# Performance work log

Measured on AMD Instinct MI355X. Metric: run time of the kernel, lower is better.

## Reference

```python
import jax, jax.numpy as jnp
import numpy as np

B, A_DIM, B_DIM, HID = 256, 128, 128, 512


def setup_inputs() -> dict:
    key = jax.random.key(0)
    ks = jax.random.split(key, 11)
    s = 0.02
    return {
        "x": jax.random.normal(ks[0], (B, A_DIM), jnp.float32),
        "y": jax.random.normal(ks[1], (B, B_DIM), jnp.float32),
        # First Linear(A+B -> H), weight split into x-part and y-part
        "Wx": jax.random.normal(ks[2], (A_DIM, HID), jnp.float32) * s,
        "Wy": jax.random.normal(ks[3], (B_DIM, HID), jnp.float32) * s,
        "b0": jax.random.normal(ks[4], (HID,), jnp.float32) * s,
        "W1": jax.random.normal(ks[5], (HID, HID), jnp.float32) * s,
        "b1": jax.random.normal(ks[6], (HID,), jnp.float32) * s,
        "W2": jax.random.normal(ks[7], (HID, HID), jnp.float32) * s,
        "b2": jax.random.normal(ks[8], (HID,), jnp.float32) * s,
        "W3": jax.random.normal(ks[9], (HID, 1), jnp.float32) * s,
        "b3": jax.random.normal(ks[10], (1,), jnp.float32) * s,
    }


def reference(x, y, Wx, Wy, b0, W1, b1, W2, b2, W3, b3):
    # Original: pair (i,j) of the *transposed* output scores f(concat(x[i], y[j])).
    # First Linear over the concat decomposes into x- and y-projections summed
    # by broadcast, avoiding the O(B^2 * (A+B)) tiled concat tensor.
    hx = x @ Wx                      # [B, H]
    hy = y @ Wy                      # [B, H]
    h = jax.nn.relu(hx[:, None, :] + hy[None, :, :] + b0)  # [B, B, H]
    h = jax.nn.relu(h @ W1 + b1)     # [B, B, H]
    h = jax.nn.relu(h @ W2 + b2)     # [B, B, H]
    scores = h @ W3 + b3             # [B, B, 1]
    return scores[..., 0]            # [B, B], out[i,j] = f(x[i], y[j])
```

## Files before the change

kernel.cpp:

```cpp
#include <hip/hip_runtime.h>
#include <hip/hip_bf16.h>

#define BSZ 256
#define ADIM 128
#define HID 512
#define MT 64
#define LDH 520

typedef __attribute__((ext_vector_type(8))) short short8;
typedef __attribute__((ext_vector_type(4))) float float4_t;

__device__ inline short f32_to_bf16_bits(float f) {
    union { float f; unsigned u; } v; v.f = f;
    unsigned u = v.u;
    unsigned r = u + 0x7FFFu + ((u >> 16) & 1u);
    return (short)(r >> 16);
}
__device__ inline float bf16_bits_to_f32(short s) {
    union { unsigned u; float f; } v;
    v.u = ((unsigned)(unsigned short)s) << 16;
    return v.f;
}

__global__ __launch_bounds__(512) void prep_kernel(
        const float* __restrict__ x, const float* __restrict__ y,
        const float* __restrict__ Wx, const float* __restrict__ Wy,
        const float* __restrict__ b0, const float* __restrict__ W1,
        const float* __restrict__ W2,
        float* __restrict__ hx, float* __restrict__ hy,
        short* __restrict__ W1p, short* __restrict__ W2p) {
    __shared__ float lds[64 * 65];
    const int tid = threadIdx.x;
    const int bid = blockIdx.x;

    if (bid < 128) {
        const bool isX = bid < 64;
        const int i0 = (isX ? bid : bid - 64) * 4;
        const float* src = isX ? x : y;
        const float* W   = isX ? Wx : Wy;
        float* dst       = isX ? hx : hy;

        lds[tid] = src[i0 * ADIM + tid];
        __syncthreads();

        const int h = tid;
        float s0 = 0.f, s1 = 0.f, s2 = 0.f, s3 = 0.f;
        const float* wcol = W + h;
        #pragma unroll 8
        for (int k = 0; k < ADIM; ++k) {
            float w = wcol[k * HID];
            s0 = fmaf(lds[k], w, s0);
            s1 = fmaf(lds[ADIM + k], w, s1);
            s2 = fmaf(lds[2 * ADIM + k], w, s2);
            s3 = fmaf(lds[3 * ADIM + k], w, s3);
        }
        float bb = isX ? b0[h] : 0.f;
        dst[(i0 + 0) * HID + h] = s0 + bb;
        dst[(i0 + 1) * HID + h] = s1 + bb;
        dst[(i0 + 2) * HID + h] = s2 + bb;
        dst[(i0 + 3) * HID + h] = s3 + bb;
    } else {
        const int tb = bid - 128;
        const bool is1 = tb < 64;
        const int t8 = is1 ? tb : tb - 64;
        const float* Wsrc = is1 ? W1 : W2;
        short* Wdst = is1 ? W1p : W2p;
        const int k0 = (t8 >> 3) * 64;
        const int n0 = (t8 & 7) * 64;

        #pragma unroll
        for (int i = 0; i < 8; ++i) {
            int r = (tid >> 6) + i * 8;
            int c = tid & 63;
            lds[c * 65 + r] = Wsrc[(k0 + r) * HID + n0 + c];
        }
        __syncthreads();

        const int local_s = tid >> 8;
        const int g_local = (tid >> 6) & 3;
        const int lane    = tid & 63;
        const int quad    = lane >> 4;
        const int lq      = lane & 15;
        const int s_glob  = (t8 >> 3) * 2 + local_s;
        const int g_glob  = (t8 & 7) * 4 + g_local;

        const float* srcp = lds + (g_local * 16 + lq) * 65 + local_s * 32 + quad * 8;
        short8 v;
        #pragma unroll
        for (int j = 0; j < 8; ++j) v[j] = f32_to_bf16_bits(srcp[j]);
        *(short8*)(Wdst + ((s_glob * 32 + g_glob) * 64 + lane) * 8) = v;
    }
}

__device__ __forceinline__ void gemm_layer(short* __restrict__ hs,
                                           const short* __restrict__ Wp,
                                           const float* __restrict__ bias,
                                           int wave, int lane) {
    const int quad = lane >> 4;
    const int lq = lane & 15;
    const int n0 = wave * 64;

    float4_t acc[4][4];
    #pragma unroll
    for (int mi = 0; mi < 4; ++mi)
        #pragma unroll
        for (int ni = 0; ni < 4; ++ni)
            acc[mi][ni] = (float4_t){0.f, 0.f, 0.f, 0.f};

    const short* pb = Wp + wave * 2048 + lane * 8;
    const short* abase = hs + lq * LDH + quad * 8;

    short8 bf[2][4];
    #pragma unroll
    for (int ni = 0; ni < 4; ++ni)
        bf[0][ni] = *(const short8*)(pb + ni * 512);

    #pragma unroll
    for (int s = 0; s < 16; ++s) {
        const int cur = s & 1;
        if (s < 15) {
            #pragma unroll
            for (int ni = 0; ni < 4; ++ni)
                bf[cur ^ 1][ni] = *(const short8*)(pb + (s + 1) * 16384 + ni * 512);
        }
        short8 af[4];
        #pragma unroll
        for (int mi = 0; mi < 4; ++mi)
            af[mi] = *(const short8*)(abase + mi * 16 * LDH + s * 32);
        #pragma unroll
        for (int mi = 0; mi < 4; ++mi)
            #pragma unroll
            for (int ni = 0; ni < 4; ++ni)
                acc[mi][ni] = __builtin_amdgcn_mfma_f32_16x16x32_bf16(
                    af[mi], bf[cur][ni], acc[mi][ni], 0, 0, 0);
    }

    float bv[4];
    #pragma unroll
    for (int ni = 0; ni < 4; ++ni) bv[ni] = bias[n0 + ni * 16 + lq];

    __syncthreads();

    #pragma unroll
    for (int ni = 0; ni < 4; ++ni) {
        #pragma unroll
        for (int mi = 0; mi < 4; ++mi) {
            #pragma unroll
            for (int r = 0; r < 4; ++r) {
                float v = acc[mi][ni][r] + bv[ni];
                v = fmaxf(v, 0.f);
                hs[(mi * 16 + quad * 4 + r) * LDH + n0 + ni * 16 + lq] = f32_to_bf16_bits(v);
            }
        }
    }
    __syncthreads();
}

__global__ __launch_bounds__(512, 4) void critic_kernel(
    const float* __restrict__ hx, const float* __restrict__ hy,
    const short* __restrict__ W1p, const short* __restrict__ W2p,
    const float* __restrict__ b1, const float* __restrict__ b2,
    const float* __restrict__ W3, const float* __restrict__ b3,
    float* __restrict__ out) {
    __shared__ short hs[MT * LDH];
    __shared__ float psum[512];

    const int tid = threadIdx.x;
    const int wave = tid >> 6;
    const int lane = tid & 63;

    const int i0 = (blockIdx.x >> 5) * 8;
    const int j0 = (blockIdx.x & 31) * 8;

    #pragma unroll
    for (int e = tid; e < MT * 64; e += 512) {
        int r = e >> 6;
        int ko = (e & 63) * 8;
        int ti = r >> 3, tj = r & 7;
        const float4_t* px = (const float4_t*)(hx + (i0 + ti) * HID + ko);
        const float4_t* py = (const float4_t*)(hy + (j0 + tj) * HID + ko);
        float4_t a0 = px[0], a1 = px[1];
        float4_t c0 = py[0], c1 = py[1];
        short8 v;
        #pragma unroll
        for (int u = 0; u < 4; ++u) v[u]     = f32_to_bf16_bits(fmaxf(a0[u] + c0[u], 0.f));
        #pragma unroll
        for (int u = 0; u < 4; ++u) v[4 + u] = f32_to_bf16_bits(fmaxf(a1[u] + c1[u], 0.f));
        *(short8*)(hs + r * LDH + ko) = v;
    }
    __syncthreads();

    gemm_layer(hs, W1p, b1, wave, lane);
    gemm_layer(hs, W2p, b2, wave, lane);

    {
        int r = tid >> 3;
        int oc = (tid & 7) * 64;
        const short* hrow = hs + r * LDH + oc;
        float s = 0.f;
        #pragma unroll
        for (int k = 0; k < 64; k += 8) {
            short8 v = *(const short8*)(hrow + k);
            #pragma unroll
            for (int u = 0; u < 8; ++u)
                s = fmaf(bf16_bits_to_f32(v[u]), W3[oc + k + u], s);
        }
        psum[tid] = s;
    }
    __syncthreads();
    if (tid < 64) {
        float s = b3[0];
        #pragma unroll
        for (int o = 0; o < 8; ++o) s += psum[tid * 8 + o];
        int ti = tid >> 3, tj = tid & 7;
        out[(i0 + ti) * BSZ + (j0 + tj)] = s;
    }
}

extern "C" void kernel_launch(void* const* d_in, const int* in_sizes, int n_in,
                              void* d_out, int out_size, void* d_ws, size_t ws_size,
                              hipStream_t stream) {
    const float* x  = (const float*)d_in[0];
    const float* y  = (const float*)d_in[1];
    const float* Wx = (const float*)d_in[2];
    const float* Wy = (const float*)d_in[3];
    const float* b0 = (const float*)d_in[4];
    const float* W1 = (const float*)d_in[5];
    const float* b1 = (const float*)d_in[6];
    const float* W2 = (const float*)d_in[7];
    const float* b2 = (const float*)d_in[8];
    const float* W3 = (const float*)d_in[9];
    const float* b3 = (const float*)d_in[10];
    float* out = (float*)d_out;

    char* ws = (char*)d_ws;
    float* hx  = (float*)(ws);
    float* hy  = (float*)(ws + 512 * 1024);
    short* W1p = (short*)(ws + 1024 * 1024);
    short* W2p = (short*)(ws + 1536 * 1024);

    prep_kernel<<<256, 512, 0, stream>>>(x, y, Wx, Wy, b0, W1, W2, hx, hy, W1p, W2p);
    critic_kernel<<<1024, 512, 0, stream>>>(hx, hy, W1p, W2p, b1, b2, W3, b3, out);
}
```

Baseline: 147.8 us.

## Use packed bf16 converts, MFMA final projection, and setprio around MFMA blocks

Replaces the software bf16 rounding with the hardware v_cvt_pk_bf16_f32 instruction in the hidden-state build and the GEMM epilogues. The W3 dot product now runs on MFMA, using a B operand that is non-zero only in column 0, and the partial sums are written to a padded psum array. The MFMA bursts are wrapped in s_setprio, the weight-prefetch pointer is strength-reduced, and prep reads x/y directly instead of staging them in LDS. Together these aim to cut VALU work in the epilogues. The final projection now multiplies W3 in bf16, which lowers its precision.

```diff
diff --git a/kernel.cpp b/kernel.cpp
--- a/kernel.cpp
+++ b/kernel.cpp
@@ -9,6 +9,7 @@
 
 typedef __attribute__((ext_vector_type(8))) short short8;
 typedef __attribute__((ext_vector_type(4))) float float4_t;
+typedef __attribute__((ext_vector_type(4))) unsigned uint4_t;
 
 __device__ inline short f32_to_bf16_bits(float f) {
     union { float f; unsigned u; } v; v.f = f;
@@ -16,10 +17,11 @@
     unsigned r = u + 0x7FFFu + ((u >> 16) & 1u);
     return (short)(r >> 16);
 }
-__device__ inline float bf16_bits_to_f32(short s) {
-    union { unsigned u; float f; } v;
-    v.u = ((unsigned)(unsigned short)s) << 16;
-    return v.f;
+
+__device__ __forceinline__ unsigned cvt_pk_bf16(float lo, float hi) {
+    unsigned r;
+    asm("v_cvt_pk_bf16_f32 %0, %1, %2" : "=v"(r) : "v"(lo), "v"(hi));
+    return r;
 }
 
 __global__ __launch_bounds__(512) void prep_kernel(
@@ -40,19 +42,17 @@
         const float* W   = isX ? Wx : Wy;
         float* dst       = isX ? hx : hy;
 
-        lds[tid] = src[i0 * ADIM + tid];
-        __syncthreads();
-
         const int h = tid;
+        const float* r0 = src + i0 * ADIM;
         float s0 = 0.f, s1 = 0.f, s2 = 0.f, s3 = 0.f;
         const float* wcol = W + h;
         #pragma unroll 8
         for (int k = 0; k < ADIM; ++k) {
             float w = wcol[k * HID];
-            s0 = fmaf(lds[k], w, s0);
-            s1 = fmaf(lds[ADIM + k], w, s1);
-            s2 = fmaf(lds[2 * ADIM + k], w, s2);
-            s3 = fmaf(lds[3 * ADIM + k], w, s3);
+            s0 = fmaf(r0[k], w, s0);
+            s1 = fmaf(r0[ADIM + k], w, s1);
+            s2 = fmaf(r0[2 * ADIM + k], w, s2);
+            s3 = fmaf(r0[3 * ADIM + k], w, s3);
         }
         float bb = isX ? b0[h] : 0.f;
         dst[(i0 + 0) * HID + h] = s0 + bb;
@@ -115,24 +115,29 @@
     for (int ni = 0; ni < 4; ++ni)
         bf[0][ni] = *(const short8*)(pb + ni * 512);
 
+    const short* ps = pb + 16384;
+
     #pragma unroll
     for (int s = 0; s < 16; ++s) {
         const int cur = s & 1;
         if (s < 15) {
             #pragma unroll
             for (int ni = 0; ni < 4; ++ni)
-                bf[cur ^ 1][ni] = *(const short8*)(pb + (s + 1) * 16384 + ni * 512);
+                bf[cur ^ 1][ni] = *(const short8*)(ps + ni * 512);
+            ps += 16384;
         }
         short8 af[4];
         #pragma unroll
         for (int mi = 0; mi < 4; ++mi)
             af[mi] = *(const short8*)(abase + mi * 16 * LDH + s * 32);
+        __builtin_amdgcn_s_setprio(1);
         #pragma unroll
         for (int mi = 0; mi < 4; ++mi)
             #pragma unroll
             for (int ni = 0; ni < 4; ++ni)
                 acc[mi][ni] = __builtin_amdgcn_mfma_f32_16x16x32_bf16(
                     af[mi], bf[cur][ni], acc[mi][ni], 0, 0, 0);
+        __builtin_amdgcn_s_setprio(0);
     }
 
     float bv[4];
@@ -145,12 +150,18 @@
     for (int ni = 0; ni < 4; ++ni) {
         #pragma unroll
         for (int mi = 0; mi < 4; ++mi) {
-            #pragma unroll
-            for (int r = 0; r < 4; ++r) {
-                float v = acc[mi][ni][r] + bv[ni];
-                v = fmaxf(v, 0.f);
-                hs[(mi * 16 + quad * 4 + r) * LDH + n0 + ni * 16 + lq] = f32_to_bf16_bits(v);
-            }
+            float v0 = fmaxf(acc[mi][ni][0] + bv[ni], 0.f);
+            float v1 = fmaxf(acc[mi][ni][1] + bv[ni], 0.f);
+            float v2 = fmaxf(acc[mi][ni][2] + bv[ni], 0.f);
+            float v3 = fmaxf(acc[mi][ni][3] + bv[ni], 0.f);
+            unsigned p01 = cvt_pk_bf16(v0, v1);
+            unsigned p23 = cvt_pk_bf16(v2, v3);
+            unsigned short* wb = (unsigned short*)hs
+                + (mi * 16 + quad * 4) * LDH + n0 + ni * 16 + lq;
+            wb[0]        = (unsigned short)p01;
+            wb[LDH]      = (unsigned short)(p01 >> 16);
+            wb[2 * LDH]  = (unsigned short)p23;
+            wb[3 * LDH]  = (unsigned short)(p23 >> 16);
         }
     }
     __syncthreads();
@@ -163,11 +174,13 @@
     const float* __restrict__ W3, const float* __restrict__ b3,
     float* __restrict__ out) {
     __shared__ short hs[MT * LDH];
-    __shared__ float psum[512];
+    __shared__ float psum[64 * 9];
 
     const int tid = threadIdx.x;
     const int wave = tid >> 6;
     const int lane = tid & 63;
+    const int quad = lane >> 4;
+    const int lq   = lane & 15;
 
     const int i0 = (blockIdx.x >> 5) * 8;
     const int j0 = (blockIdx.x & 31) * 8;
@@ -181,12 +194,11 @@
         const float4_t* py = (const float4_t*)(hy + (j0 + tj) * HID + ko);
         float4_t a0 = px[0], a1 = px[1];
         float4_t c0 = py[0], c1 = py[1];
-        short8 v;
-        #pragma unroll
-        for (int u = 0; u < 4; ++u) v[u]     = f32_to_bf16_bits(fmaxf(a0[u] + c0[u], 0.f));
-        #pragma unroll
-        for (int u = 0; u < 4; ++u) v[4 + u] = f32_to_bf16_bits(fmaxf(a1[u] + c1[u], 0.f));
-        *(short8*)(hs + r * LDH + ko) = v;
+        unsigned d0 = cvt_pk_bf16(fmaxf(a0[0] + c0[0], 0.f), fmaxf(a0[1] + c0[1], 0.f));
+        unsigned d1 = cvt_pk_bf16(fmaxf(a0[2] + c0[2], 0.f), fmaxf(a0[3] + c0[3], 0.f));
+        unsigned d2 = cvt_pk_bf16(fmaxf(a1[0] + c1[0], 0.f), fmaxf(a1[1] + c1[1], 0.f));
+        unsigned d3 = cvt_pk_bf16(fmaxf(a1[2] + c1[2], 0.f), fmaxf(a1[3] + c1[3], 0.f));
+        *(uint4_t*)(hs + r * LDH + ko) = (uint4_t){d0, d1, d2, d3};
     }
     __syncthreads();
 
@@ -194,26 +206,47 @@
     gemm_layer(hs, W2p, b2, wave, lane);
 
     {
-        int r = tid >> 3;
-        int oc = (tid & 7) * 64;
-        const short* hrow = hs + r * LDH + oc;
-        float s = 0.f;
-        #pragma unroll
-        for (int k = 0; k < 64; k += 8) {
-            short8 v = *(const short8*)(hrow + k);
-            #pragma unroll
-            for (int u = 0; u < 8; ++u)
-                s = fmaf(bf16_bits_to_f32(v[u]), W3[oc + k + u], s);
-        }
-        psum[tid] = s;
+        const int n0 = wave * 64;
+        union { unsigned u[4]; short8 v; } w3u[2];
+        #pragma unroll
+        for (int s = 0; s < 2; ++s) {
+            float wv[8];
+            #pragma unroll
+            for (int j = 0; j < 8; ++j)
+                wv[j] = (lq == 0) ? W3[n0 + s * 32 + quad * 8 + j] : 0.f;
+            #pragma unroll
+            for (int j = 0; j < 4; ++j)
+                w3u[s].u[j] = cvt_pk_bf16(wv[2 * j], wv[2 * j + 1]);
+        }
+
+        float4_t facc[4];
+        #pragma unroll
+        for (int mi = 0; mi < 4; ++mi) facc[mi] = (float4_t){0.f, 0.f, 0.f, 0.f};
+
+        const short* abase = hs + lq * LDH + n0 + quad * 8;
+        #pragma unroll
+        for (int s = 0; s < 2; ++s)
+            #pragma unroll
+            for (int mi = 0; mi < 4; ++mi) {
+                short8 af = *(const short8*)(abase + mi * 16 * LDH + s * 32);
+                facc[mi] = __builtin_amdgcn_mfma_f32_16x16x32_bf16(
+                    af, w3u[s].v, facc[mi], 0, 0, 0);
+            }
+
+        if (lq == 0) {
+            #pragma unroll
+            for (int mi = 0; mi < 4; ++mi)
+                #pragma unroll
+                for (int r = 0; r < 4; ++r)
+                    psum[(mi * 16 + quad * 4 + r) * 9 + wave] = facc[mi][r];
+        }
     }
     __syncthreads();
     if (tid < 64) {
         float s = b3[0];
         #pragma unroll
-        for (int o = 0; o < 8; ++o) s += psum[tid * 8 + o];
-        int ti = tid >> 3, tj = tid & 7;
-        out[(i0 + ti) * BSZ + (j0 + tj)] = s;
+        for (int o = 0; o < 8; ++o) s += psum[tid * 9 + o];
+        out[(i0 + (tid >> 3)) * BSZ + (j0 + (tid & 7))] = s;
     }
 }
 
```

New measurement: 137.5 us. -6.9%, faster.
